# Performance work log

Hardware: AMD Instinct MI355X
Metric: run time of the kernel (lower is better)

The kernel has to match this reference:

```python
import jax, jax.numpy as jnp
import numpy as np

D_MODEL = 1024
N_HEAD = 16
SEG = 256
HEAD_DIM = D_MODEL // N_HEAD  # 64; only used as softmax scale (module never splits heads)
SCALE = 1.0 / (HEAD_DIM ** 0.5)


def setup_inputs() -> dict:
    key = jax.random.key(0)
    ks = jax.random.split(key, 9)
    B, L, D = 4, 4096, D_MODEL
    s = 1.0 / np.sqrt(D)
    x = jax.random.normal(ks[0], (B, L, D), dtype=jnp.float32)
    Wq = jax.random.uniform(ks[1], (D, D), jnp.float32, -s, s)
    bq = jax.random.uniform(ks[2], (D,), jnp.float32, -s, s)
    Wk = jax.random.uniform(ks[3], (D, D), jnp.float32, -s, s)
    bk = jax.random.uniform(ks[4], (D,), jnp.float32, -s, s)
    Wv = jax.random.uniform(ks[5], (D, D), jnp.float32, -s, s)
    bv = jax.random.uniform(ks[6], (D,), jnp.float32, -s, s)
    Wo = jax.random.uniform(ks[7], (D, D), jnp.float32, -s, s)
    bo = jax.random.uniform(ks[8], (D,), jnp.float32, -s, s)
    return {"x": x, "Wq": Wq, "bq": bq, "Wk": Wk, "bk": bk,
            "Wv": Wv, "bv": bv, "Wo": Wo, "bo": bo}


def reference(x, Wq, bq, Wk, bk, Wv, bv, Wo, bo):
    B, L, D = x.shape
    n_seg = L // SEG
    xs = x.reshape(B, n_seg, SEG, D)  # [B, n, S, D] block-diagonal segments

    # Local (per-segment) attention, batched over all segments at once.
    Q = jnp.einsum('bnsd,ed->bnse', xs, Wq) + bq
    K = jnp.einsum('bnsd,ed->bnse', xs, Wk) + bk
    V = jnp.einsum('bnsd,ed->bnse', xs, Wv) + bv
    scores = jnp.einsum('bnse,bnte->bnst', Q, K) * SCALE  # [B, n, S, S]
    attn = jax.nn.softmax(scores, axis=-1)
    local = jnp.einsum('bnst,bnte->bnse', attn, V)  # [B, n, S, D]

    # Global attention over segment summaries (first token of each segment).
    summ = xs[:, :, 0, :]  # [B, n, D]
    Qg = jnp.einsum('bnd,ed->bne', summ, Wq) + bq
    Kg = jnp.einsum('bnd,ed->bne', summ, Wk) + bk
    Vg = jnp.einsum('bnd,ed->bne', summ, Wv) + bv
    scores_g = jnp.einsum('bne,bme->bnm', Qg, Kg) * SCALE  # [B, n, n]
    attn_g = jax.nn.softmax(scores_g, axis=-1)
    global_out = jnp.einsum('bnm,bme->bne', attn_g, Vg)  # [B, n, D]

    # Broadcast each segment's global summary over its tokens and add.
    out = local + global_out[:, :, None, :]  # [B, n, S, D]
    out = out.reshape(B, L, D)
    return jnp.einsum('bld,ed->ble', out, Wo) + bo
```

## Files before the change

### kernel.cpp

```cpp
#include <hip/hip_runtime.h>
#include <hip/hip_bf16.h>
#include <stdint.h>

typedef unsigned short u16;
typedef __attribute__((ext_vector_type(8))) short s16x8;
typedef __attribute__((ext_vector_type(4))) float f32x4;

__device__ __forceinline__ u16 f2bf(float f){
  uint32_t u = __builtin_bit_cast(uint32_t, f);
  u += 0x7FFFu + ((u >> 16) & 1u);
  return (u16)(u >> 16);
}
__device__ __forceinline__ float bf2f(u16 h){
  uint32_t u = ((uint32_t)h) << 16;
  return __builtin_bit_cast(float, u);
}
__device__ __forceinline__ void gl_lds16(const void* g, void* l){
  __builtin_amdgcn_global_load_lds((__attribute__((address_space(1))) void*)g,
                                   (__attribute__((address_space(3))) void*)l,
                                   16, 0, 0);
}

#define MROWS 16384
#define DMODEL 1024
#define NQKV 3072
#define NSEGS 64
#define O_XB    0u
#define O_WQKV  33554432u
#define O_WO    39845888u
#define O_BQKV  41943040u
#define O_QKV   41955328u
#define O_VT    142618624u
#define O_GOUT  176173056u
#define O_GPR   176435200u

__global__ __launch_bounds__(256) void pack_kernel(
    const float* __restrict__ x,
    const float* __restrict__ wq, const float* __restrict__ wk,
    const float* __restrict__ wv, const float* __restrict__ wo,
    const float* __restrict__ bq, const float* __restrict__ bk, const float* __restrict__ bv,
    u16* __restrict__ xb, u16* __restrict__ wqkvb, u16* __restrict__ wob,
    float* __restrict__ bqkv)
{
  const int stride = gridDim.x * 256;
  const int gid = blockIdx.x * 256 + threadIdx.x;
  if(gid < 3072)
    bqkv[gid] = (gid < 1024) ? bq[gid] : (gid < 2048 ? bk[gid - 1024] : bv[gid - 2048]);
  for(int q = gid; q < 4194304; q += stride){
    float4 v = *(const float4*)(x + (size_t)q * 4);
    ushort4 o; o.x = f2bf(v.x); o.y = f2bf(v.y); o.z = f2bf(v.z); o.w = f2bf(v.w);
    *(ushort4*)(xb + (size_t)q * 4) = o;
  }
  for(int q = gid; q < 786432; q += stride){
    int elem = q << 2;
    int m = elem >> 20;
    const float* s = (m == 0) ? wq : (m == 1 ? wk : wv);
    float4 v = *(const float4*)(s + (elem & 1048575));
    ushort4 o; o.x = f2bf(v.x); o.y = f2bf(v.y); o.z = f2bf(v.z); o.w = f2bf(v.w);
    *(ushort4*)(wqkvb + elem) = o;
  }
  for(int q = gid; q < 262144; q += stride){
    float4 v = *(const float4*)(wo + (size_t)q * 4);
    ushort4 o; o.x = f2bf(v.x); o.y = f2bf(v.y); o.z = f2bf(v.z); o.w = f2bf(v.w);
    *(ushort4*)(wob + (size_t)q * 4) = o;
  }
}

template<bool OUT_BF16>
__global__ __launch_bounds__(512, 2) void gemm256_kernel(
    const u16* __restrict__ A, const u16* __restrict__ Bt,
    const float* __restrict__ bias, void* __restrict__ Cv,
    const int K, const int ldc, const int ncb)
{
  __shared__ char sm[131072];
  const int tid = threadIdx.x;
  const int wv = tid >> 6, lane = tid & 63;
  const int l15 = lane & 15, l4 = lane >> 4;
  const int wr = wv >> 2, wc = wv & 3;

  const int nwg = (int)gridDim.x;
  int bid = (int)blockIdx.x;
  bid = (bid & 7) * (nwg >> 3) + (bid >> 3);
  const int brow = (bid / ncb) << 8, bcol = (bid % ncb) << 8;

  int offA[8], offB[4];
#pragma unroll
  for(int m = 0; m < 8; ++m){
    int row = wr * 128 + m * 16 + l15;
    offA[m] = row * 64 + ((l4 ^ ((row >> 1) & 3)) << 4);
  }
#pragma unroll
  for(int n = 0; n < 4; ++n){
    int row = wc * 64 + n * 16 + l15;
    offB[n] = 16384 + row * 64 + ((l4 ^ ((row >> 1) & 3)) << 4);
  }

  const u16* srcA[2]; const u16* srcB[2]; int dstOff[2];
#pragma unroll
  for(int r = 0; r < 2; ++r){
    int off = r * 8192 + tid * 16;
    int row = off >> 6, g = (off >> 4) & 3;
    int gs = g ^ ((row >> 1) & 3);
    srcA[r] = A  + (size_t)(brow + row) * K + gs * 8;
    srcB[r] = Bt + (size_t)(bcol + row) * K + gs * 8;
    dstOff[r] = r * 8192 + wv * 1024;
  }

#define STAGE256(kt_, buf_) do{                                   \
    char* base_ = sm + (buf_) * 32768;                            \
    const int ko_ = (kt_) << 5;                                   \
    gl_lds16(srcA[0] + ko_, base_ + dstOff[0]);                   \
    gl_lds16(srcA[1] + ko_, base_ + dstOff[1]);                   \
    gl_lds16(srcB[0] + ko_, base_ + 16384 + dstOff[0]);           \
    gl_lds16(srcB[1] + ko_, base_ + 16384 + dstOff[1]);           \
  }while(0)

  const f32x4 fz = {0.f, 0.f, 0.f, 0.f};
  f32x4 acc[8][4];
#pragma unroll
  for(int m = 0; m < 8; ++m)
#pragma unroll
    for(int n = 0; n < 4; ++n) acc[m][n] = fz;

  const int nkt = K >> 5;
  STAGE256(0, 0); STAGE256(1, 1); STAGE256(2, 2);

  for(int kt = 0; kt < nkt; ++kt){
    const int rem = nkt - 1 - kt;
    if(rem >= 2)      asm volatile("s_waitcnt vmcnt(8)" ::: "memory");
    else if(rem == 1) asm volatile("s_waitcnt vmcnt(4)" ::: "memory");
    else              asm volatile("s_waitcnt vmcnt(0)" ::: "memory");
    __builtin_amdgcn_s_barrier();
    asm volatile("" ::: "memory");
    if(kt + 3 < nkt) STAGE256(kt + 3, (kt + 3) & 3);

    char* cb = sm + (kt & 3) * 32768;
    s16x8 b[4], a[4];
#pragma unroll
    for(int n = 0; n < 4; ++n) b[n] = *(const s16x8*)(cb + offB[n]);
#pragma unroll
    for(int m = 0; m < 4; ++m) a[m] = *(const s16x8*)(cb + offA[m]);
    __builtin_amdgcn_s_setprio(1);
#pragma unroll
    for(int m = 0; m < 4; ++m)
#pragma unroll
      for(int n = 0; n < 4; ++n)
        acc[m][n] = __builtin_amdgcn_mfma_f32_16x16x32_bf16(a[m], b[n], acc[m][n], 0, 0, 0);
    __builtin_amdgcn_s_setprio(0);
#pragma unroll
    for(int m = 0; m < 4; ++m) a[m] = *(const s16x8*)(cb + offA[m + 4]);
    __builtin_amdgcn_s_setprio(1);
#pragma unroll
    for(int m = 0; m < 4; ++m)
#pragma unroll
      for(int n = 0; n < 4; ++n)
        acc[m + 4][n] = __builtin_amdgcn_mfma_f32_16x16x32_bf16(a[m], b[n], acc[m + 4][n], 0, 0, 0);
    __builtin_amdgcn_s_setprio(0);
  }
#undef STAGE256

  float bvv[4];
#pragma unroll
  for(int n = 0; n < 4; ++n) bvv[n] = bias[bcol + wc * 64 + n * 16 + l15];
#pragma unroll
  for(int m = 0; m < 8; ++m)
#pragma unroll
    for(int n = 0; n < 4; ++n)
#pragma unroll
      for(int r = 0; r < 4; ++r){
        const int row = brow + wr * 128 + m * 16 + (l4 << 2) + r;
        const int col = bcol + wc * 64 + n * 16 + l15;
        const float v = acc[m][n][r] + bvv[n];
        if constexpr(OUT_BF16) ((u16*)Cv)[(size_t)row * ldc + col] = f2bf(v);
        else                   ((float*)Cv)[(size_t)row * ldc + col] = v;
      }
}

__global__ __launch_bounds__(512, 4) void gemm128_kernel(
    const u16* __restrict__ A, const u16* __restrict__ Bt,
    const float* __restrict__ bias, float* __restrict__ C,
    const int K, const int ldc, const int ncb)
{
  __shared__ char sm[73728];
  const int tid = threadIdx.x;
  const int wv = tid >> 6, lane = tid & 63;
  const int l15 = lane & 15, l4 = lane >> 4;
  const int wr = wv >> 2, wc = wv & 3;

  const int nwg = (int)gridDim.x;
  int bid = (int)blockIdx.x;
  bid = (bid & 7) * (nwg >> 3) + (bid >> 3);
  const int brow = (bid / ncb) << 8, bcol = (bid % ncb) << 7;

  int offA[8], offB[2];
#pragma unroll
  for(int m = 0; m < 8; ++m){
    int row = wr * 128 + m * 16 + l15;
    offA[m] = row * 64 + ((l4 ^ ((row >> 1) & 3)) << 4);
  }
#pragma unroll
  for(int n = 0; n < 2; ++n){
    int row = wc * 32 + n * 16 + l15;
    offB[n] = 16384 + row * 64 + ((l4 ^ ((row >> 1) & 3)) << 4);
  }

  const u16* srcA[2]; const u16* srcB; int dstOff[2];
#pragma unroll
  for(int r = 0; r < 2; ++r){
    int off = r * 8192 + tid * 16;
    int row = off >> 6, g = (off >> 4) & 3;
    int gs = g ^ ((row >> 1) & 3);
    srcA[r] = A + (size_t)(brow + row) * K + gs * 8;
    dstOff[r] = r * 8192 + wv * 1024;
  }
  {
    int off = tid * 16;
    int row = off >> 6, g = (off >> 4) & 3;
    int gs = g ^ ((row >> 1) & 3);
    srcB = Bt + (size_t)(bcol + row) * K + gs * 8;
  }

#define STAGE128(kt_, buf_) do{                                   \
    char* base_ = sm + (buf_) * 24576;                            \
    const int ko_ = (kt_) << 5;                                   \
    gl_lds16(srcA[0] + ko_, base_ + dstOff[0]);                   \
    gl_lds16(srcA[1] + ko_, base_ + dstOff[1]);                   \
    gl_lds16(srcB + ko_, base_ + 16384 + wv * 1024);              \
  }while(0)

  const f32x4 fz = {0.f, 0.f, 0.f, 0.f};
  f32x4 acc[8][2];
#pragma unroll
  for(int m = 0; m < 8; ++m)
#pragma unroll
    for(int n = 0; n < 2; ++n) acc[m][n] = fz;

  const int nkt = K >> 5;
  STAGE128(0, 0); STAGE128(1, 1);
  int cur = 0;
  for(int kt = 0; kt < nkt; ++kt){
    if(kt + 1 < nkt) asm volatile("s_waitcnt vmcnt(3)" ::: "memory");
    else             asm volatile("s_waitcnt vmcnt(0)" ::: "memory");
    __builtin_amdgcn_s_barrier();
    asm volatile("" ::: "memory");
    if(kt + 2 < nkt){
      int nb = cur + 2; if(nb >= 3) nb -= 3;
      STAGE128(kt + 2, nb);
    }
    char* cb = sm + cur * 24576;
    s16x8 b[2], a[4];
#pragma unroll
    for(int n = 0; n < 2; ++n) b[n] = *(const s16x8*)(cb + offB[n]);
#pragma unroll
    for(int m = 0; m < 4; ++m) a[m] = *(const s16x8*)(cb + offA[m]);
    __builtin_amdgcn_s_setprio(1);
#pragma unroll
    for(int m = 0; m < 4; ++m)
#pragma unroll
      for(int n = 0; n < 2; ++n)
        acc[m][n] = __builtin_amdgcn_mfma_f32_16x16x32_bf16(a[m], b[n], acc[m][n], 0, 0, 0);
    __builtin_amdgcn_s_setprio(0);
#pragma unroll
    for(int m = 0; m < 4; ++m) a[m] = *(const s16x8*)(cb + offA[m + 4]);
    __builtin_amdgcn_s_setprio(1);
#pragma unroll
    for(int m = 0; m < 4; ++m)
#pragma unroll
      for(int n = 0; n < 2; ++n)
        acc[m + 4][n] = __builtin_amdgcn_mfma_f32_16x16x32_bf16(a[m], b[n], acc[m + 4][n], 0, 0, 0);
    __builtin_amdgcn_s_setprio(0);
    if(++cur == 3) cur = 0;
  }
#undef STAGE128

  float bvv[2];
#pragma unroll
  for(int n = 0; n < 2; ++n) bvv[n] = bias[bcol + wc * 32 + n * 16 + l15];
#pragma unroll
  for(int m = 0; m < 8; ++m)
#pragma unroll
    for(int n = 0; n < 2; ++n)
#pragma unroll
      for(int r = 0; r < 4; ++r){
        const int row = brow + wr * 128 + m * 16 + (l4 << 2) + r;
        const int col = bcol + wc * 32 + n * 16 + l15;
        C[(size_t)row * ldc + col] = acc[m][n][r] + bvv[n];
      }
}

__global__ __launch_bounds__(256) void transpose_v_kernel(
    const u16* __restrict__ QKV, u16* __restrict__ Vt)
{
  __shared__ u16 tile[64 * 65];
  const int bid = blockIdx.x;
  const int seg = bid >> 6, t = bid & 63;
  const int t0 = (t >> 4) << 6;
  const int e0 = (t & 15) << 6;
  const int tid = threadIdx.x;
#pragma unroll
  for(int i = 0; i < 16; ++i){
    int idx = i * 256 + tid; int r = idx >> 6, c = idx & 63;
    tile[r * 65 + c] = QKV[((size_t)seg * 256 + t0 + r) * NQKV + 2048 + e0 + c];
  }
  __syncthreads();
#pragma unroll
  for(int i = 0; i < 16; ++i){
    int idx = i * 256 + tid; int r = idx >> 6, c = idx & 63;
    Vt[((size_t)seg * 1024 + e0 + r) * 256 + t0 + c] = tile[c * 65 + r];
  }
}

__global__ __launch_bounds__(256) void gscore_kernel(
    const u16* __restrict__ QKV, float* __restrict__ gpr)
{
  __shared__ float sc[16];
  const int b = blockIdx.x >> 4, i = blockIdx.x & 15;
  const int tid = threadIdx.x;
  const int j = tid >> 4, slice = tid & 15;
  const u16* qp = QKV + (size_t)(b * 16 + i) * 256 * NQKV + slice * 64;
  const u16* kp = QKV + (size_t)(b * 16 + j) * 256 * NQKV + 1024 + slice * 64;
  float acc = 0.f;
#pragma unroll
  for(int c = 0; c < 8; ++c){
    s16x8 qv = *(const s16x8*)(qp + c * 8);
    s16x8 kv = *(const s16x8*)(kp + c * 8);
#pragma unroll
    for(int e = 0; e < 8; ++e) acc += bf2f((u16)qv[e]) * bf2f((u16)kv[e]);
  }
#pragma unroll
  for(int off = 8; off >= 1; off >>= 1) acc += __shfl_xor(acc, off, 64);
  if(slice == 0) sc[j] = acc * 0.125f;
  __syncthreads();
  if(tid < 16){
    float v = sc[tid];
    float m = v;
#pragma unroll
    for(int off = 8; off >= 1; off >>= 1) m = fmaxf(m, __shfl_xor(m, off, 64));
    float p = __expf(v - m);
    float s = p;
#pragma unroll
    for(int off = 8; off >= 1; off >>= 1) s += __shfl_xor(s, off, 64);
    gpr[(size_t)b * 256 + i * 16 + tid] = p / s;
  }
}

__global__ __launch_bounds__(256) void gpv_kernel(
    const u16* __restrict__ QKV, const float* __restrict__ gpr,
    float* __restrict__ gout)
{
  __shared__ float spr[256];
  const int b = blockIdx.x >> 4, ch = blockIdx.x & 15;
  const int tid = threadIdx.x;
  spr[tid] = gpr[(size_t)b * 256 + tid];
  __syncthreads();
  const int e = (ch << 6) + (tid & 63);
  const int ng = tid >> 6;
  const u16* vp = QKV + (size_t)(b * 16) * 256 * NQKV + 2048 + e;
  float o0 = 0.f, o1 = 0.f, o2 = 0.f, o3 = 0.f;
#pragma unroll
  for(int m = 0; m < 16; ++m){
    float v = bf2f(vp[(size_t)m * 256 * NQKV]);
    o0 += spr[(ng * 4 + 0) * 16 + m] * v;
    o1 += spr[(ng * 4 + 1) * 16 + m] * v;
    o2 += spr[(ng * 4 + 2) * 16 + m] * v;
    o3 += spr[(ng * 4 + 3) * 16 + m] * v;
  }
  gout[((size_t)b * 16 + ng * 4 + 0) * 1024 + e] = o0;
  gout[((size_t)b * 16 + ng * 4 + 1) * 1024 + e] = o1;
  gout[((size_t)b * 16 + ng * 4 + 2) * 1024 + e] = o2;
  gout[((size_t)b * 16 + ng * 4 + 3) * 1024 + e] = o3;
}

__global__ __launch_bounds__(512, 2) void attn_local_kernel(
    const u16* __restrict__ QKV, const u16* __restrict__ Vt,
    const float* __restrict__ gout, u16* __restrict__ AO)
{
  __shared__ char sm[131072];
  float* smax = (float*)(sm + 32768);
  float* ssum = (float*)(sm + 33792);
  const int tid = threadIdx.x;
  const int wv = tid >> 6, lane = tid & 63;
  const int l15 = lane & 15, l4 = lane >> 4;
  const int wr = wv >> 2, wc = wv & 3;
  int bid = (int)blockIdx.x;
  bid = (bid & 7) * 32 + (bid >> 3);
  const int seg = bid >> 2, rt = bid & 3;
  const int r0 = rt << 6;
  const size_t segQ = (size_t)seg * 256 * NQKV;

  const int offq = wv * 1024 + lane * 16;
  const int dstQ = wv * 1024;
  const int qrow = offq >> 7;
  const int qgs  = ((offq >> 4) & 7) ^ (qrow & 7);
  const u16* qsrc = QKV + segQ + (size_t)(r0 + qrow) * NQKV + qgs * 8;
  const u16* ksrc[4];
  const u16* vsrc[4];
#pragma unroll
  for(int c = 0; c < 4; ++c){
    int off = c * 8192 + offq;
    int row = off >> 7;
    int gs  = ((off >> 4) & 7) ^ (row & 7);
    ksrc[c] = QKV + segQ + (size_t)row * NQKV + 1024 + gs * 8;
    vsrc[c] = Vt + (size_t)seg * 262144 + (size_t)row * 256 + gs * 8;
  }

#define STAGE_P1(d0_, base_) do{                                        \
    gl_lds16(qsrc + (d0_), sm + (base_) + dstQ);                        \
    _Pragma("unroll")                                                   \
    for(int c_ = 0; c_ < 4; ++c_)                                       \
      gl_lds16(ksrc[c_] + (d0_), sm + (base_) + 8192 + c_ * 8192 + dstQ); \
  }while(0)
#define STAGE_V(j_, vb_) do{                                            \
    const int vo_ = ((j_) >> 2) * 65536 + ((j_) & 3) * 64;              \
    _Pragma("unroll")                                                   \
    for(int c_ = 0; c_ < 4; ++c_)                                       \
      gl_lds16(vsrc[c_] + vo_, sm + 32768 + (vb_) * 32768 + c_ * 8192 + dstQ); \
  }while(0)

  int aOff[2][2], bOff[4][2];
#pragma unroll
  for(int m = 0; m < 2; ++m){
    int row = wr * 32 + m * 16 + l15;
#pragma unroll
    for(int kk = 0; kk < 2; ++kk)
      aOff[m][kk] = row * 128 + ((kk * 64 + l4 * 16) ^ ((row & 7) << 4));
  }
#pragma unroll
  for(int n = 0; n < 4; ++n){
    int row = wc * 64 + n * 16 + l15;
#pragma unroll
    for(int kk = 0; kk < 2; ++kk)
      bOff[n][kk] = 8192 + row * 128 + ((kk * 64 + l4 * 16) ^ ((row & 7) << 4));
  }

  const f32x4 fz = {0.f, 0.f, 0.f, 0.f};
  f32x4 acc1[2][4];
#pragma unroll
  for(int m = 0; m < 2; ++m)
#pragma unroll
    for(int n = 0; n < 4; ++n) acc1[m][n] = fz;

  STAGE_P1(0, 0); STAGE_P1(64, 40960);
  asm volatile("s_waitcnt vmcnt(5)" ::: "memory");
  __builtin_amdgcn_s_barrier();
  asm volatile("" ::: "memory");
  int cur = 0;
  for(int dt = 0; dt < 16; ++dt){
    const int base = cur * 40960;
    if(dt + 2 < 16){
      int nb = cur + 2; if(nb >= 3) nb -= 3;
      STAGE_P1((dt + 2) << 6, nb * 40960);
    }
    s16x8 a[2][2], b[4][2];
#pragma unroll
    for(int m = 0; m < 2; ++m)
#pragma unroll
      for(int kk = 0; kk < 2; ++kk) a[m][kk] = *(const s16x8*)(sm + base + aOff[m][kk]);
#pragma unroll
    for(int n = 0; n < 4; ++n)
#pragma unroll
      for(int kk = 0; kk < 2; ++kk) b[n][kk] = *(const s16x8*)(sm + base + bOff[n][kk]);
    __builtin_amdgcn_s_setprio(1);
#pragma unroll
    for(int kk = 0; kk < 2; ++kk)
#pragma unroll
      for(int m = 0; m < 2; ++m)
#pragma unroll
        for(int n = 0; n < 4; ++n)
          acc1[m][n] = __builtin_amdgcn_mfma_f32_16x16x32_bf16(a[m][kk], b[n][kk], acc1[m][n], 0, 0, 0);
    __builtin_amdgcn_s_setprio(0);
    if(dt + 2 < 16) asm volatile("s_waitcnt vmcnt(5) lgkmcnt(0)" ::: "memory");
    else            asm volatile("s_waitcnt vmcnt(0) lgkmcnt(0)" ::: "memory");
    __builtin_amdgcn_s_barrier();
    asm volatile("" ::: "memory");
    if(++cur == 3) cur = 0;
  }

  const float CE = 0.18033688011112042f;
#pragma unroll
  for(int m = 0; m < 2; ++m)
#pragma unroll
    for(int r = 0; r < 4; ++r){
      float v = -1e30f;
#pragma unroll
      for(int n = 0; n < 4; ++n) v = fmaxf(v, acc1[m][n][r]);
#pragma unroll
      for(int off = 8; off >= 1; off >>= 1) v = fmaxf(v, __shfl_xor(v, off, 64));
      if(l15 == 0) smax[wc * 64 + wr * 32 + m * 16 + (l4 << 2) + r] = v;
    }
  asm volatile("s_waitcnt lgkmcnt(0)" ::: "memory");
  __builtin_amdgcn_s_barrier();
  asm volatile("" ::: "memory");
#pragma unroll
  for(int m = 0; m < 2; ++m)
#pragma unroll
    for(int r = 0; r < 4; ++r){
      const int idx = wr * 32 + m * 16 + (l4 << 2) + r;
      const float g = fmaxf(fmaxf(smax[idx], smax[64 + idx]),
                            fmaxf(smax[128 + idx], smax[192 + idx]));
      float s = 0.f;
#pragma unroll
      for(int n = 0; n < 4; ++n){
        float p = exp2f((acc1[m][n][r] - g) * CE);
        acc1[m][n][r] = p;
        s += p;
      }
#pragma unroll
      for(int off = 8; off >= 1; off >>= 1) s += __shfl_xor(s, off, 64);
      if(l15 == 0) ssum[wc * 64 + idx] = s;
    }
  asm volatile("s_waitcnt lgkmcnt(0)" ::: "memory");
  __builtin_amdgcn_s_barrier();
  asm volatile("" ::: "memory");
  float inv2[2][4];
#pragma unroll
  for(int m = 0; m < 2; ++m)
#pragma unroll
    for(int r = 0; r < 4; ++r){
      const int idx = wr * 32 + m * 16 + (l4 << 2) + r;
      inv2[m][r] = 1.f / (ssum[idx] + ssum[64 + idx] + ssum[128 + idx] + ssum[192 + idx]);
    }
#pragma unroll
  for(int m = 0; m < 2; ++m)
#pragma unroll
    for(int n = 0; n < 4; ++n)
#pragma unroll
      for(int r = 0; r < 4; ++r){
        const int rr = wr * 32 + m * 16 + (l4 << 2) + r;
        const int t  = wc * 64 + n * 16 + l15;
        *(u16*)(sm + rr * 512 + ((t << 1) ^ ((rr & 7) << 4))) = f2bf(acc1[m][n][r] * inv2[m][r]);
      }
  asm volatile("s_waitcnt lgkmcnt(0)" ::: "memory");
  __builtin_amdgcn_s_barrier();
  asm volatile("" ::: "memory");

  int prow[2], pswz[2];
#pragma unroll
  for(int m = 0; m < 2; ++m){
    int row = wr * 32 + m * 16 + l15;
    prow[m] = row * 512;
    pswz[m] = (row & 7) << 4;
  }
  int vOff[4][2];
#pragma unroll
  for(int n = 0; n < 4; ++n){
    int row = wc * 64 + n * 16 + l15;
#pragma unroll
    for(int kk = 0; kk < 2; ++kk)
      vOff[n][kk] = row * 128 + ((kk * 64 + l4 * 16) ^ ((row & 7) << 4));
  }

  STAGE_V(0, 0); STAGE_V(1, 1);
  asm volatile("s_waitcnt vmcnt(4)" ::: "memory");
  __builtin_amdgcn_s_barrier();
  asm volatile("" ::: "memory");
  f32x4 acc2[2][4];
  int cv = 0;
  for(int j = 0; j < 16; ++j){
    const int ts = j & 3, ns = j >> 2;
    if(ts == 0){
#pragma unroll
      for(int m = 0; m < 2; ++m)
#pragma unroll
        for(int n = 0; n < 4; ++n) acc2[m][n] = fz;
    }
    if(j + 2 < 16){
      int nb = cv + 2; if(nb >= 3) nb -= 3;
      STAGE_V(j + 2, nb);
    }
    char* vbase = sm + 32768 + cv * 32768;
    s16x8 a[2][2], b[4][2];
#pragma unroll
    for(int m = 0; m < 2; ++m)
#pragma unroll
      for(int kk = 0; kk < 2; ++kk)
        a[m][kk] = *(const s16x8*)(sm + prow[m] + (((ts << 7) + (kk << 6) + (l4 << 4)) ^ pswz[m]));
#pragma unroll
    for(int n = 0; n < 4; ++n)
#pragma unroll
      for(int kk = 0; kk < 2; ++kk) b[n][kk] = *(const s16x8*)(vbase + vOff[n][kk]);
    __builtin_amdgcn_s_setprio(1);
#pragma unroll
    for(int kk = 0; kk < 2; ++kk)
#pragma unroll
      for(int m = 0; m < 2; ++m)
#pragma unroll
        for(int n = 0; n < 4; ++n)
          acc2[m][n] = __builtin_amdgcn_mfma_f32_16x16x32_bf16(a[m][kk], b[n][kk], acc2[m][n], 0, 0, 0);
    __builtin_amdgcn_s_setprio(0);
    if(j + 2 < 16) asm volatile("s_waitcnt vmcnt(4) lgkmcnt(0)" ::: "memory");
    else           asm volatile("s_waitcnt vmcnt(0) lgkmcnt(0)" ::: "memory");
    __builtin_amdgcn_s_barrier();
    asm volatile("" ::: "memory");
    if(++cv == 3) cv = 0;

    if(ts == 3){
      float gv[4];
#pragma unroll
      for(int n = 0; n < 4; ++n)
        gv[n] = gout[(size_t)seg * 1024 + ns * 256 + wc * 64 + n * 16 + l15];
#pragma unroll
      for(int m = 0; m < 2; ++m)
#pragma unroll
        for(int n = 0; n < 4; ++n)
#pragma unroll
          for(int r = 0; r < 4; ++r){
            const int row = r0 + wr * 32 + m * 16 + (l4 << 2) + r;
            const int e   = ns * 256 + wc * 64 + n * 16 + l15;
            AO[((size_t)seg * 256 + row) * 1024 + e] = f2bf(acc2[m][n][r] + gv[n]);
          }
    }
  }
#undef STAGE_P1
#undef STAGE_V
}

extern "C" void kernel_launch(void* const* d_in, const int* in_sizes, int n_in,
                              void* d_out, int out_size, void* d_ws, size_t ws_size,
                              hipStream_t stream)
{
  const float* x  = (const float*)d_in[0];
  const float* Wq = (const float*)d_in[1];
  const float* bq = (const float*)d_in[2];
  const float* Wk = (const float*)d_in[3];
  const float* bk = (const float*)d_in[4];
  const float* Wv = (const float*)d_in[5];
  const float* bv = (const float*)d_in[6];
  const float* Wo = (const float*)d_in[7];
  const float* bo = (const float*)d_in[8];

  char* ws = (char*)d_ws;
  u16*   xb    = (u16*)(ws + O_XB);
  u16*   wqkvb = (u16*)(ws + O_WQKV);
  u16*   wob   = (u16*)(ws + O_WO);
  float* bqkv  = (float*)(ws + O_BQKV);
  u16*   qkv   = (u16*)(ws + O_QKV);
  u16*   vt    = (u16*)(ws + O_VT);
  float* gout  = (float*)(ws + O_GOUT);
  float* gpr   = (float*)(ws + O_GPR);
  u16*   ao    = xb;

  pack_kernel<<<4096, 256, 0, stream>>>(x, Wq, Wk, Wv, Wo, bq, bk, bv, xb, wqkvb, wob, bqkv);
  gemm256_kernel<true><<<dim3((NQKV / 256) * (MROWS / 256)), 512, 0, stream>>>(
      xb, wqkvb, bqkv, qkv, DMODEL, NQKV, NQKV / 256);
  transpose_v_kernel<<<NSEGS * 64, 256, 0, stream>>>(qkv, vt);
  gscore_kernel<<<64, 256, 0, stream>>>(qkv, gpr);
  gpv_kernel<<<64, 256, 0, stream>>>(qkv, gpr, gout);
  attn_local_kernel<<<256, 512, 0, stream>>>(qkv, vt, gout, ao);
  gemm128_kernel<<<dim3((DMODEL / 128) * (MROWS / 256)), 512, 0, stream>>>(
      ao, wob, bo, (float*)d_out, DMODEL, DMODEL, DMODEL / 128);
}
```

Before: 230.4 us.

## Rework 256x256 GEMM into BK=64 double-buffered, quadrant-interleaved pipeline; drop gemm128

Restructures the 256x256 bf16 GEMM kernel to use K-tiles of 64 with two 64KB LDS buffers and a new 8-way XOR swizzle. Each iteration is split into four MFMA quadrants, with LDS fragment reads and global-to-LDS prefetches of A and B interleaved between barriers, so loads overlap compute more finely. The output projection now uses this kernel with 256-wide N tiles instead of the separate 128-wide kernel. This adds many more barriers per iteration and 128KB of LDS per block, which limits occupancy. The output-projection grid is also halved.

```diff
diff --git a/kernel.cpp b/kernel.cpp
--- a/kernel.cpp
+++ b/kernel.cpp
@@ -83,37 +83,37 @@
   bid = (bid & 7) * (nwg >> 3) + (bid >> 3);
   const int brow = (bid / ncb) << 8, bcol = (bid % ncb) << 8;
 
-  int offA[8], offB[4];
+  int aOff[8][2], bOff[4][2];
 #pragma unroll
   for(int m = 0; m < 8; ++m){
     int row = wr * 128 + m * 16 + l15;
-    offA[m] = row * 64 + ((l4 ^ ((row >> 1) & 3)) << 4);
+#pragma unroll
+    for(int kk = 0; kk < 2; ++kk)
+      aOff[m][kk] = row * 128 + ((kk * 64 + l4 * 16) ^ ((row & 7) << 4));
   }
 #pragma unroll
   for(int n = 0; n < 4; ++n){
     int row = wc * 64 + n * 16 + l15;
-    offB[n] = 16384 + row * 64 + ((l4 ^ ((row >> 1) & 3)) << 4);
-  }
-
-  const u16* srcA[2]; const u16* srcB[2]; int dstOff[2];
-#pragma unroll
-  for(int r = 0; r < 2; ++r){
+#pragma unroll
+    for(int kk = 0; kk < 2; ++kk)
+      bOff[n][kk] = 32768 + row * 128 + ((kk * 64 + l4 * 16) ^ ((row & 7) << 4));
+  }
+
+  const u16* srcA[4]; const u16* srcB[4]; int dstOff[4];
+#pragma unroll
+  for(int r = 0; r < 4; ++r){
     int off = r * 8192 + tid * 16;
-    int row = off >> 6, g = (off >> 4) & 3;
-    int gs = g ^ ((row >> 1) & 3);
+    int row = off >> 7;
+    int gs  = ((off >> 4) & 7) ^ (row & 7);
     srcA[r] = A  + (size_t)(brow + row) * K + gs * 8;
     srcB[r] = Bt + (size_t)(bcol + row) * K + gs * 8;
     dstOff[r] = r * 8192 + wv * 1024;
   }
 
-#define STAGE256(kt_, buf_) do{                                   \
-    char* base_ = sm + (buf_) * 32768;                            \
-    const int ko_ = (kt_) << 5;                                   \
-    gl_lds16(srcA[0] + ko_, base_ + dstOff[0]);                   \
-    gl_lds16(srcA[1] + ko_, base_ + dstOff[1]);                   \
-    gl_lds16(srcB[0] + ko_, base_ + 16384 + dstOff[0]);           \
-    gl_lds16(srcB[1] + ko_, base_ + 16384 + dstOff[1]);           \
-  }while(0)
+#define STAGE_A64(kt_, buf_) do{ char* b_ = sm + (buf_) * 65536; const int ko_ = (kt_) << 6; \
+    _Pragma("unroll") for(int r_ = 0; r_ < 4; ++r_) gl_lds16(srcA[r_] + ko_, b_ + dstOff[r_]); }while(0)
+#define STAGE_B64(kt_, buf_) do{ char* b_ = sm + (buf_) * 65536 + 32768; const int ko_ = (kt_) << 6; \
+    _Pragma("unroll") for(int r_ = 0; r_ < 4; ++r_) gl_lds16(srcB[r_] + ko_, b_ + dstOff[r_]); }while(0)
 
   const f32x4 fz = {0.f, 0.f, 0.f, 0.f};
   f32x4 acc[8][4];
@@ -122,42 +122,101 @@
 #pragma unroll
     for(int n = 0; n < 4; ++n) acc[m][n] = fz;
 
-  const int nkt = K >> 5;
-  STAGE256(0, 0); STAGE256(1, 1); STAGE256(2, 2);
+  const int nkt = K >> 6;
+  STAGE_A64(0, 0); STAGE_B64(0, 0);
+  STAGE_A64(1, 1); STAGE_B64(1, 1);
+  asm volatile("s_waitcnt vmcnt(8)" ::: "memory");
+  __builtin_amdgcn_s_barrier();
+  asm volatile("" ::: "memory");
 
   for(int kt = 0; kt < nkt; ++kt){
-    const int rem = nkt - 1 - kt;
-    if(rem >= 2)      asm volatile("s_waitcnt vmcnt(8)" ::: "memory");
-    else if(rem == 1) asm volatile("s_waitcnt vmcnt(4)" ::: "memory");
-    else              asm volatile("s_waitcnt vmcnt(0)" ::: "memory");
-    __builtin_amdgcn_s_barrier();
-    asm volatile("" ::: "memory");
-    if(kt + 3 < nkt) STAGE256(kt + 3, (kt + 3) & 3);
-
-    char* cb = sm + (kt & 3) * 32768;
-    s16x8 b[4], a[4];
-#pragma unroll
-    for(int n = 0; n < 4; ++n) b[n] = *(const s16x8*)(cb + offB[n]);
-#pragma unroll
-    for(int m = 0; m < 4; ++m) a[m] = *(const s16x8*)(cb + offA[m]);
+    char* cb = sm + (kt & 1) * 65536;
+    const bool pf = (kt + 2 < nkt);
+    const int pb = kt & 1;
+    s16x8 aF[4][2], bL[2][2], bH[2][2];
+
+#pragma unroll
+    for(int n = 0; n < 2; ++n)
+#pragma unroll
+      for(int kk = 0; kk < 2; ++kk) bL[n][kk] = *(const s16x8*)(cb + bOff[n][kk]);
+#pragma unroll
+    for(int m = 0; m < 4; ++m)
+#pragma unroll
+      for(int kk = 0; kk < 2; ++kk) aF[m][kk] = *(const s16x8*)(cb + aOff[m][kk]);
+    asm volatile("s_waitcnt lgkmcnt(8)" ::: "memory");
+    __builtin_amdgcn_s_barrier();
+    asm volatile("s_waitcnt lgkmcnt(0)" ::: "memory");
     __builtin_amdgcn_s_setprio(1);
 #pragma unroll
+    for(int kk = 0; kk < 2; ++kk)
+#pragma unroll
+      for(int m = 0; m < 4; ++m)
+#pragma unroll
+        for(int n = 0; n < 2; ++n)
+          acc[m][n] = __builtin_amdgcn_mfma_f32_16x16x32_bf16(aF[m][kk], bL[n][kk], acc[m][n], 0, 0, 0);
+    __builtin_amdgcn_s_setprio(0);
+    __builtin_amdgcn_s_barrier();
+    asm volatile("" ::: "memory");
+
+#pragma unroll
+    for(int n = 0; n < 2; ++n)
+#pragma unroll
+      for(int kk = 0; kk < 2; ++kk) bH[n][kk] = *(const s16x8*)(cb + bOff[n + 2][kk]);
+    __builtin_amdgcn_s_barrier();
+    asm volatile("s_waitcnt lgkmcnt(0)" ::: "memory");
+    __builtin_amdgcn_s_setprio(1);
+#pragma unroll
+    for(int kk = 0; kk < 2; ++kk)
+#pragma unroll
+      for(int m = 0; m < 4; ++m)
+#pragma unroll
+        for(int n = 0; n < 2; ++n)
+          acc[m][n + 2] = __builtin_amdgcn_mfma_f32_16x16x32_bf16(aF[m][kk], bH[n][kk], acc[m][n + 2], 0, 0, 0);
+    __builtin_amdgcn_s_setprio(0);
+    __builtin_amdgcn_s_barrier();
+    asm volatile("" ::: "memory");
+
+#pragma unroll
     for(int m = 0; m < 4; ++m)
 #pragma unroll
-      for(int n = 0; n < 4; ++n)
-        acc[m][n] = __builtin_amdgcn_mfma_f32_16x16x32_bf16(a[m], b[n], acc[m][n], 0, 0, 0);
+      for(int kk = 0; kk < 2; ++kk) aF[m][kk] = *(const s16x8*)(cb + aOff[m + 4][kk]);
+    if(pf) STAGE_B64(kt + 2, pb);
+    __builtin_amdgcn_s_barrier();
+    asm volatile("s_waitcnt lgkmcnt(0)" ::: "memory");
+    __builtin_amdgcn_s_setprio(1);
+#pragma unroll
+    for(int kk = 0; kk < 2; ++kk)
+#pragma unroll
+      for(int m = 0; m < 4; ++m)
+#pragma unroll
+        for(int n = 0; n < 2; ++n)
+          acc[m + 4][n + 2] = __builtin_amdgcn_mfma_f32_16x16x32_bf16(aF[m][kk], bH[n][kk], acc[m + 4][n + 2], 0, 0, 0);
     __builtin_amdgcn_s_setprio(0);
-#pragma unroll
-    for(int m = 0; m < 4; ++m) a[m] = *(const s16x8*)(cb + offA[m + 4]);
+    __builtin_amdgcn_s_barrier();
+    asm volatile("" ::: "memory");
+
+    if(pf){
+      STAGE_A64(kt + 2, pb);
+      asm volatile("s_waitcnt vmcnt(8)" ::: "memory");
+    } else if(kt + 1 < nkt){
+      asm volatile("s_waitcnt vmcnt(0)" ::: "memory");
+    }
+    __builtin_amdgcn_s_barrier();
+    asm volatile("" ::: "memory");
     __builtin_amdgcn_s_setprio(1);
 #pragma unroll
-    for(int m = 0; m < 4; ++m)
-#pragma unroll
-      for(int n = 0; n < 4; ++n)
-        acc[m + 4][n] = __builtin_amdgcn_mfma_f32_16x16x32_bf16(a[m], b[n], acc[m + 4][n], 0, 0, 0);
+    for(int kk = 0; kk < 2; ++kk)
+#pragma unroll
+      for(int m = 0; m < 4; ++m)
+#pragma unroll
+        for(int n = 0; n < 2; ++n)
+          acc[m + 4][n] = __builtin_amdgcn_mfma_f32_16x16x32_bf16(aF[m][kk], bL[n][kk], acc[m + 4][n], 0, 0, 0);
     __builtin_amdgcn_s_setprio(0);
-  }
-#undef STAGE256
+    __builtin_amdgcn_s_barrier();
+    asm volatile("" ::: "memory");
+  }
+#undef STAGE_A64
+#undef STAGE_B64
 
   float bvv[4];
 #pragma unroll
@@ -173,118 +232,6 @@
         const float v = acc[m][n][r] + bvv[n];
         if constexpr(OUT_BF16) ((u16*)Cv)[(size_t)row * ldc + col] = f2bf(v);
         else                   ((float*)Cv)[(size_t)row * ldc + col] = v;
-      }
-}
-
-__global__ __launch_bounds__(512, 4) void gemm128_kernel(
-    const u16* __restrict__ A, const u16* __restrict__ Bt,
-    const float* __restrict__ bias, float* __restrict__ C,
-    const int K, const int ldc, const int ncb)
-{
-  __shared__ char sm[73728];
-  const int tid = threadIdx.x;
-  const int wv = tid >> 6, lane = tid & 63;
-  const int l15 = lane & 15, l4 = lane >> 4;
-  const int wr = wv >> 2, wc = wv & 3;
-
-  const int nwg = (int)gridDim.x;
-  int bid = (int)blockIdx.x;
-  bid = (bid & 7) * (nwg >> 3) + (bid >> 3);
-  const int brow = (bid / ncb) << 8, bcol = (bid % ncb) << 7;
-
-  int offA[8], offB[2];
-#pragma unroll
-  for(int m = 0; m < 8; ++m){
-    int row = wr * 128 + m * 16 + l15;
-    offA[m] = row * 64 + ((l4 ^ ((row >> 1) & 3)) << 4);
-  }
-#pragma unroll
-  for(int n = 0; n < 2; ++n){
-    int row = wc * 32 + n * 16 + l15;
-    offB[n] = 16384 + row * 64 + ((l4 ^ ((row >> 1) & 3)) << 4);
-  }
-
-  const u16* srcA[2]; const u16* srcB; int dstOff[2];
-#pragma unroll
-  for(int r = 0; r < 2; ++r){
-    int off = r * 8192 + tid * 16;
-    int row = off >> 6, g = (off >> 4) & 3;
-    int gs = g ^ ((row >> 1) & 3);
-    srcA[r] = A + (size_t)(brow + row) * K + gs * 8;
-    dstOff[r] = r * 8192 + wv * 1024;
-  }
-  {
-    int off = tid * 16;
-    int row = off >> 6, g = (off >> 4) & 3;
-    int gs = g ^ ((row >> 1) & 3);
-    srcB = Bt + (size_t)(bcol + row) * K + gs * 8;
-  }
-
-#define STAGE128(kt_, buf_) do{                                   \
-    char* base_ = sm + (buf_) * 24576;                            \
-    const int ko_ = (kt_) << 5;                                   \
-    gl_lds16(srcA[0] + ko_, base_ + dstOff[0]);                   \
-    gl_lds16(srcA[1] + ko_, base_ + dstOff[1]);                   \
-    gl_lds16(srcB + ko_, base_ + 16384 + wv * 1024);              \
-  }while(0)
-
-  const f32x4 fz = {0.f, 0.f, 0.f, 0.f};
-  f32x4 acc[8][2];
-#pragma unroll
-  for(int m = 0; m < 8; ++m)
-#pragma unroll
-    for(int n = 0; n < 2; ++n) acc[m][n] = fz;
-
-  const int nkt = K >> 5;
-  STAGE128(0, 0); STAGE128(1, 1);
-  int cur = 0;
-  for(int kt = 0; kt < nkt; ++kt){
-    if(kt + 1 < nkt) asm volatile("s_waitcnt vmcnt(3)" ::: "memory");
-    else             asm volatile("s_waitcnt vmcnt(0)" ::: "memory");
-    __builtin_amdgcn_s_barrier();
-    asm volatile("" ::: "memory");
-    if(kt + 2 < nkt){
-      int nb = cur + 2; if(nb >= 3) nb -= 3;
-      STAGE128(kt + 2, nb);
-    }
-    char* cb = sm + cur * 24576;
-    s16x8 b[2], a[4];
-#pragma unroll
-    for(int n = 0; n < 2; ++n) b[n] = *(const s16x8*)(cb + offB[n]);
-#pragma unroll
-    for(int m = 0; m < 4; ++m) a[m] = *(const s16x8*)(cb + offA[m]);
-    __builtin_amdgcn_s_setprio(1);
-#pragma unroll
-    for(int m = 0; m < 4; ++m)
-#pragma unroll
-      for(int n = 0; n < 2; ++n)
-        acc[m][n] = __builtin_amdgcn_mfma_f32_16x16x32_bf16(a[m], b[n], acc[m][n], 0, 0, 0);
-    __builtin_amdgcn_s_setprio(0);
-#pragma unroll
-    for(int m = 0; m < 4; ++m) a[m] = *(const s16x8*)(cb + offA[m + 4]);
-    __builtin_amdgcn_s_setprio(1);
-#pragma unroll
-    for(int m = 0; m < 4; ++m)
-#pragma unroll
-      for(int n = 0; n < 2; ++n)
-        acc[m + 4][n] = __builtin_amdgcn_mfma_f32_16x16x32_bf16(a[m], b[n], acc[m + 4][n], 0, 0, 0);
-    __builtin_amdgcn_s_setprio(0);
-    if(++cur == 3) cur = 0;
-  }
-#undef STAGE128
-
-  float bvv[2];
-#pragma unroll
-  for(int n = 0; n < 2; ++n) bvv[n] = bias[bcol + wc * 32 + n * 16 + l15];
-#pragma unroll
-  for(int m = 0; m < 8; ++m)
-#pragma unroll
-    for(int n = 0; n < 2; ++n)
-#pragma unroll
-      for(int r = 0; r < 4; ++r){
-        const int row = brow + wr * 128 + m * 16 + (l4 << 2) + r;
-        const int col = bcol + wc * 32 + n * 16 + l15;
-        C[(size_t)row * ldc + col] = acc[m][n][r] + bvv[n];
       }
 }
 
@@ -647,6 +594,6 @@
   gscore_kernel<<<64, 256, 0, stream>>>(qkv, gpr);
   gpv_kernel<<<64, 256, 0, stream>>>(qkv, gpr, gout);
   attn_local_kernel<<<256, 512, 0, stream>>>(qkv, vt, gout, ao);
-  gemm128_kernel<<<dim3((DMODEL / 128) * (MROWS / 256)), 512, 0, stream>>>(
-      ao, wob, bo, (float*)d_out, DMODEL, DMODEL, DMODEL / 128);
-}
+  gemm256_kernel<false><<<dim3((DMODEL / 256) * (MROWS / 256)), 512, 0, stream>>>(
+      ao, wob, bo, d_out, DMODEL, DMODEL, DMODEL / 256);
+}
```

Result: no change. 233.5 us (+1.4%).
